# Optimization experiments

Hardware: AMD Instinct MI355X
Metric: run time of the kernel (lower is better)

Reference implementation:

```python
import jax, jax.numpy as jnp
import numpy as np

IN_F = 256
OUT_F = 128
ALPHA = 0.02  # LeakyReLU negative slope
NEG_INF = -9e15


def setup_inputs() -> dict:
    key = jax.random.key(0)
    ks = jax.random.split(key, 6)
    N = 8192
    x = jax.random.normal(ks[0], (N, IN_F), dtype=jnp.float32)
    adj = jax.random.randint(ks[1], (N, N), 0, 2, dtype=jnp.int32)
    # nn.Linear(in_feature, out_feature)
    lim1 = 1.0 / np.sqrt(IN_F)
    W1 = jax.random.uniform(ks[2], (IN_F, OUT_F), minval=-lim1, maxval=lim1, dtype=jnp.float32)
    b1 = jax.random.uniform(ks[3], (OUT_F,), minval=-lim1, maxval=lim1, dtype=jnp.float32)
    # nn.Linear(2*out_feature, 1)
    lim2 = 1.0 / np.sqrt(2 * OUT_F)
    a = jax.random.uniform(ks[4], (2 * OUT_F,), minval=-lim2, maxval=lim2, dtype=jnp.float32)
    b_att = jax.random.uniform(ks[5], (), minval=-lim2, maxval=lim2, dtype=jnp.float32)
    return {"x": x, "adj": adj, "W1": W1, "b1": b1, "a": a, "b_att": b_att}


def reference(x, adj, W1, b1, a, b_att):
    # Wh = weight1(x)  -> [N, F_out]
    Wh = x @ W1 + b1
    # att(cat(Wh_i, Wh_j)) = Wh_i @ a[:F] + Wh_j @ a[F:] + b  (no N^2*2F tensor)
    f_src = Wh @ a[:OUT_F]   # [N]
    f_dst = Wh @ a[OUT_F:]   # [N]
    e = f_src[:, None] + f_dst[None, :] + b_att          # [N, N]
    e = jnp.where(e > 0, e, ALPHA * e)                    # LeakyReLU
    scores = jnp.where(adj > 0, e, NEG_INF)
    attention = jax.nn.softmax(scores, axis=1)            # [N, N]
    # dropout is identity in eval mode (training=False)
    h_prime = attention @ Wh                               # [N, F_out]
    return jax.nn.elu(h_prime)                             # concat=True
```

## Files before the change

### kernel.cpp

```cpp
#include <hip/hip_runtime.h>
#include <hip/hip_bf16.h>

#define NODES 8192
#define INF_ 256
#define OUTF 128
#define LRALPHA 0.02f

typedef __bf16 bf16;
typedef bf16 bf16x4 __attribute__((ext_vector_type(4)));
typedef bf16 bf16x8 __attribute__((ext_vector_type(8)));
typedef float f32x4 __attribute__((ext_vector_type(4)));
typedef float f32x16 __attribute__((ext_vector_type(16)));
typedef int i32x4 __attribute__((ext_vector_type(4)));

__global__ __launch_bounds__(256) void gat_prep_r2(
    const float* __restrict__ x, const float* __restrict__ W1,
    const float* __restrict__ b1, const float* __restrict__ a,
    const float* __restrict__ b_att,
    bf16* __restrict__ WhbT, float* __restrict__ fsb, float* __restrict__ E1,
    float* __restrict__ E2, float* __restrict__ fd, float* __restrict__ F1,
    float* __restrict__ F2)
{
    __shared__ float xsT[64][36];
    __shared__ float ws1[64][132];
    __shared__ float wh[32][128];

    const int t = threadIdx.x;
    const int rbase = blockIdx.x * 32;
    const int tr = t >> 5;
    const int tc = t & 31;

    f32x4 acc[4];
    f32x4 bias = *(const f32x4*)&b1[tc * 4];
#pragma unroll
    for (int i = 0; i < 4; ++i) acc[i] = bias;

    for (int kt = 0; kt < 4; ++kt) {
        const int kb = kt * 64;
        {
            int r = t >> 3;
            int kq = (t & 7) * 8;
            f32x4 v0 = *(const f32x4*)&x[(size_t)(rbase + r) * INF_ + kb + kq];
            f32x4 v1 = *(const f32x4*)&x[(size_t)(rbase + r) * INF_ + kb + kq + 4];
#pragma unroll
            for (int i = 0; i < 4; ++i) xsT[kq + i][r] = v0[i];
#pragma unroll
            for (int i = 0; i < 4; ++i) xsT[kq + 4 + i][r] = v1[i];
        }
        {
            int kr = t >> 2;
            int cq = (t & 3) * 32;
#pragma unroll
            for (int i = 0; i < 8; ++i) {
                f32x4 v = *(const f32x4*)&W1[(size_t)(kb + kr) * OUTF + cq + i * 4];
                *(f32x4*)&ws1[kr][cq + i * 4] = v;
            }
        }
        __syncthreads();
        for (int kk = 0; kk < 64; ++kk) {
            f32x4 xa = *(const f32x4*)&xsT[kk][tr * 4];
            f32x4 wb = *(const f32x4*)&ws1[kk][tc * 4];
#pragma unroll
            for (int i = 0; i < 4; ++i)
#pragma unroll
                for (int j = 0; j < 4; ++j)
                    acc[i][j] += xa[i] * wb[j];
        }
        __syncthreads();
    }

#pragma unroll
    for (int i = 0; i < 4; ++i)
        *(f32x4*)&wh[tr * 4 + i][tc * 4] = acc[i];
    __syncthreads();

    if (t < 32) {
        float s1 = 0.f, s2 = 0.f;
        for (int c = 0; c < OUTF; ++c) {
            float v = wh[t][c];
            s1 += v * a[c];
            s2 += v * a[OUTF + c];
        }
        float fsv = s1 + b_att[0];
        int r = rbase + t;
        fsb[r] = fsv;
        E1[r] = expf(fsv);
        E2[r] = expf(LRALPHA * fsv);
        fd[r] = s2;
        F1[r] = expf(s2);
        F2[r] = expf(LRALPHA * s2);
    }

    {
        int c = t >> 1;
        int rr = (t & 1) * 16;
        bf16x8 b0, b1v;
#pragma unroll
        for (int i = 0; i < 8; ++i) b0[i] = (bf16)wh[rr + i][c];
#pragma unroll
        for (int i = 0; i < 8; ++i) b1v[i] = (bf16)wh[rr + 8 + i][c];
        *(bf16x8*)&WhbT[(size_t)c * NODES + rbase + rr] = b0;
        *(bf16x8*)&WhbT[(size_t)c * NODES + rbase + rr + 8] = b1v;
    }
}

#define SOFT_BAR() do { asm volatile("s_waitcnt lgkmcnt(0)" ::: "memory"); \
                        __builtin_amdgcn_s_barrier(); } while (0)

__global__ __launch_bounds__(1024, 4) void gat_attn_r2(
    const int* __restrict__ adj,
    const bf16* __restrict__ WhbT,
    const float* __restrict__ fsb, const float* __restrict__ E1,
    const float* __restrict__ E2, const float* __restrict__ fd,
    const float* __restrict__ F1, const float* __restrict__ F2,
    float* __restrict__ out)
{
    extern __shared__ char smem[];
    const int tid = threadIdx.x;
    const int wv = tid >> 6;
    const int lane = tid & 63;
    const int jg = wv >> 2;
    const int tt = wv & 3;
    const int rbase = blockIdx.x * 32;

    char* wbufA = smem + (jg * 2) * 4096;
    char* wbufB = smem + (jg * 2 + 1) * 4096;
    float* denred = (float*)(smem + 49152);

    const int r8 = lane >> 3;
    const int c8 = lane & 7;
    const int wrow = tt * 8 + r8;
    const int arow = lane & 31;
    const int ag = lane >> 5;

    const int gr = rbase + wrow;
    const float fsbv = fsb[gr];
    const float e1v = E1[gr];
    const float e2v = E2[gr];

    f32x16 acc;
#pragma unroll
    for (int i = 0; i < 16; ++i) acc[i] = 0.f;
    float den = 0.f;

    const int jw0 = jg * (NODES / 4);
    const size_t adj_row = (size_t)gr * NODES;
    const size_t whb_row = (size_t)(32 * tt + arow) * NODES;

    auto compute_w = [&](char* buf, int jb, i32x4 a0, i32x4 a1) {
        f32x4 fd0 = *(const f32x4*)&fd[jb + c8 * 8];
        f32x4 fd1 = *(const f32x4*)&fd[jb + c8 * 8 + 4];
        f32x4 g10 = *(const f32x4*)&F1[jb + c8 * 8];
        f32x4 g11 = *(const f32x4*)&F1[jb + c8 * 8 + 4];
        f32x4 g20 = *(const f32x4*)&F2[jb + c8 * 8];
        f32x4 g21 = *(const f32x4*)&F2[jb + c8 * 8 + 4];
        bf16x8 wb;
#pragma unroll
        for (int jj = 0; jj < 4; ++jj) {
            float s = fsbv + fd0[jj];
            bool pos = s > 0.f;
            float w = (pos ? e1v : e2v) * (pos ? g10[jj] : g20[jj]);
            w = a0[jj] ? w : 0.f;
            den += w;
            wb[jj] = (bf16)w;
        }
#pragma unroll
        for (int jj = 0; jj < 4; ++jj) {
            float s = fsbv + fd1[jj];
            bool pos = s > 0.f;
            float w = (pos ? e1v : e2v) * (pos ? g11[jj] : g21[jj]);
            w = a1[jj] ? w : 0.f;
            den += w;
            wb[4 + jj] = (bf16)w;
        }
        const int off = (wrow * 128 + c8 * 16) ^ ((wrow & 7) << 4);
        *(bf16x8*)(buf + off) = wb;
    };

    auto do_mfma = [&](const char* buf, int jb) {
        bf16x8 bfr[4];
#pragma unroll
        for (int m = 0; m < 4; ++m)
            bfr[m] = *(const bf16x8*)&WhbT[whb_row + jb + 16 * m + 8 * ag];
        bf16x8 af[4];
#pragma unroll
        for (int m = 0; m < 4; ++m) {
            const int aoff = (arow * 128 + m * 32 + ag * 16) ^ ((arow & 7) << 4);
            af[m] = *(const bf16x8*)(buf + aoff);
        }
#pragma unroll
        for (int m = 0; m < 4; ++m)
            acc = __builtin_amdgcn_mfma_f32_32x32x16_bf16(af[m], bfr[m], acc, 0, 0, 0);
    };

    i32x4 a0 = *(const i32x4*)&adj[adj_row + jw0 + c8 * 8];
    i32x4 a1 = *(const i32x4*)&adj[adj_row + jw0 + c8 * 8 + 4];
    i32x4 b0 = *(const i32x4*)&adj[adj_row + jw0 + 64 + c8 * 8];
    i32x4 b1 = *(const i32x4*)&adj[adj_row + jw0 + 64 + c8 * 8 + 4];
    compute_w(wbufA, jw0, a0, a1);
    SOFT_BAR();

    char* cur = wbufA;
    char* nxt = wbufB;
#pragma unroll 2
    for (int p = 0; p < 32; ++p) {
        const int jb = jw0 + p * 64;
        const int pc = (p + 2 <= 31) ? (p + 2) : 31;
        i32x4 n0 = *(const i32x4*)&adj[adj_row + jw0 + pc * 64 + c8 * 8];
        i32x4 n1 = *(const i32x4*)&adj[adj_row + jw0 + pc * 64 + c8 * 8 + 4];
        if (p < 31) compute_w(nxt, jb + 64, b0, b1);
        do_mfma(cur, jb);
        SOFT_BAR();
        b0 = n0; b1 = n1;
        char* tmp = cur; cur = nxt; nxt = tmp;
    }

    den += __shfl_xor(den, 1);
    den += __shfl_xor(den, 2);
    den += __shfl_xor(den, 4);
    if (c8 == 0) denred[jg * 32 + wrow] = den;

    if (jg > 0) {
        float* z = (float*)(smem + (size_t)((jg - 1) * 4 + tt) * 4096) + lane * 16;
        *(f32x16*)z = acc;
    }
    __syncthreads();

    if (jg == 0) {
#pragma unroll
        for (int q = 0; q < 3; ++q) {
            const float* z = (const float*)(smem + (size_t)(q * 4 + tt) * 4096) + lane * 16;
            f32x16 v = *(const f32x16*)z;
#pragma unroll
            for (int i = 0; i < 16; ++i) acc[i] += v[i];
        }
#pragma unroll
        for (int rg = 0; rg < 16; ++rg) {
            const int row = (rg & 3) + 8 * (rg >> 2) + 4 * ag;
            float ds = denred[row] + denred[32 + row] + denred[64 + row] + denred[96 + row];
            float v = acc[rg] / ds;
            v = v > 0.f ? v : expm1f(v);
            out[(size_t)(rbase + row) * OUTF + 32 * tt + arow] = v;
        }
    }
}

extern "C" void kernel_launch(void* const* d_in, const int* in_sizes, int n_in,
                              void* d_out, int out_size, void* d_ws, size_t ws_size,
                              hipStream_t stream) {
    const float* x     = (const float*)d_in[0];
    const int*   adj   = (const int*)d_in[1];
    const float* W1    = (const float*)d_in[2];
    const float* b1    = (const float*)d_in[3];
    const float* a     = (const float*)d_in[4];
    const float* b_att = (const float*)d_in[5];
    float* out = (float*)d_out;

    char* ws = (char*)d_ws;
    bf16* WhbT = (bf16*)ws;
    float* fsb = (float*)(ws + (size_t)2 * 1024 * 1024);
    float* E1 = fsb + NODES;
    float* E2 = E1 + NODES;
    float* fd = E2 + NODES;
    float* F1 = fd + NODES;
    float* F2 = F1 + NODES;

    hipLaunchKernelGGL(gat_prep_r2, dim3(NODES / 32), dim3(256), 0, stream,
                       x, W1, b1, a, b_att, WhbT, fsb, E1, E2, fd, F1, F2);

    const size_t smem2 = 49152 + 512;
    hipLaunchKernelGGL(gat_attn_r2, dim3(NODES / 32), dim3(1024), smem2, stream,
                       adj, WhbT, fsb, E1, E2, fd, F1, F2, out);
}
```

Measured before the change: 138.0 us.

## Stage F1/F2 tables in LDS, drop fd via algebra, prefetch WhbT fragments

```diff
diff --git a/kernel.cpp b/kernel.cpp
--- a/kernel.cpp
+++ b/kernel.cpp
@@ -13,7 +13,7 @@
 typedef float f32x16 __attribute__((ext_vector_type(16)));
 typedef int i32x4 __attribute__((ext_vector_type(4)));
 
-__global__ __launch_bounds__(256) void gat_prep_r2(
+__global__ __launch_bounds__(256) void gat_prep_r3(
     const float* __restrict__ x, const float* __restrict__ W1,
     const float* __restrict__ b1, const float* __restrict__ a,
     const float* __restrict__ b_att,
@@ -107,25 +107,41 @@
 #define SOFT_BAR() do { asm volatile("s_waitcnt lgkmcnt(0)" ::: "memory"); \
                         __builtin_amdgcn_s_barrier(); } while (0)
 
-__global__ __launch_bounds__(1024, 4) void gat_attn_r2(
+#define WBUF_OFF   0
+#define DENRED_OFF 32768
+#define F1T_OFF    33280
+#define F2T_OFF    66048
+#define ZONE_OFF   33280
+#define SMEM2_SIZE 98816
+
+__global__ __launch_bounds__(1024, 4) void gat_attn_r3(
     const int* __restrict__ adj,
     const bf16* __restrict__ WhbT,
     const float* __restrict__ fsb, const float* __restrict__ E1,
-    const float* __restrict__ E2, const float* __restrict__ fd,
+    const float* __restrict__ E2,
     const float* __restrict__ F1, const float* __restrict__ F2,
     float* __restrict__ out)
 {
     extern __shared__ char smem[];
     const int tid = threadIdx.x;
+    const int lane = tid & 63;
     const int wv = tid >> 6;
-    const int lane = tid & 63;
     const int jg = wv >> 2;
     const int tt = wv & 3;
     const int rbase = blockIdx.x * 32;
 
-    char* wbufA = smem + (jg * 2) * 4096;
-    char* wbufB = smem + (jg * 2 + 1) * 4096;
-    float* denred = (float*)(smem + 49152);
+    char* wbufA = smem + WBUF_OFF + (jg * 2) * 4096;
+    char* wbufB = smem + WBUF_OFF + (jg * 2 + 1) * 4096;
+    float* denred = (float*)(smem + DENRED_OFF);
+    float* F1t = (float*)(smem + F1T_OFF);
+    float* F2t = (float*)(smem + F2T_OFF);
+
+#pragma unroll
+    for (int it = 0; it < 2; ++it) {
+        int i = (it * 1024 + tid) * 4;
+        *(f32x4*)&F1t[i] = *(const f32x4*)&F1[i];
+        *(f32x4*)&F2t[i] = *(const f32x4*)&F2[i];
+    }
 
     const int r8 = lane >> 3;
     const int c8 = lane & 7;
@@ -147,56 +163,43 @@
     const size_t adj_row = (size_t)gr * NODES;
     const size_t whb_row = (size_t)(32 * tt + arow) * NODES;
 
+    __syncthreads();
+
     auto compute_w = [&](char* buf, int jb, i32x4 a0, i32x4 a1) {
-        f32x4 fd0 = *(const f32x4*)&fd[jb + c8 * 8];
-        f32x4 fd1 = *(const f32x4*)&fd[jb + c8 * 8 + 4];
-        f32x4 g10 = *(const f32x4*)&F1[jb + c8 * 8];
-        f32x4 g11 = *(const f32x4*)&F1[jb + c8 * 8 + 4];
-        f32x4 g20 = *(const f32x4*)&F2[jb + c8 * 8];
-        f32x4 g21 = *(const f32x4*)&F2[jb + c8 * 8 + 4];
+        const int cb = jb + c8 * 8;
+        f32x4 g10 = *(const f32x4*)&F1t[cb];
+        f32x4 g11 = *(const f32x4*)&F1t[cb + 4];
+        f32x4 g20 = *(const f32x4*)&F2t[cb];
+        f32x4 g21 = *(const f32x4*)&F2t[cb + 4];
         bf16x8 wb;
 #pragma unroll
         for (int jj = 0; jj < 4; ++jj) {
-            float s = fsbv + fd0[jj];
-            bool pos = s > 0.f;
-            float w = (pos ? e1v : e2v) * (pos ? g10[jj] : g20[jj]);
+            float t = e1v * g10[jj];
+            float w = t > 1.f ? t : e2v * g20[jj];
             w = a0[jj] ? w : 0.f;
             den += w;
             wb[jj] = (bf16)w;
         }
 #pragma unroll
         for (int jj = 0; jj < 4; ++jj) {
-            float s = fsbv + fd1[jj];
-            bool pos = s > 0.f;
-            float w = (pos ? e1v : e2v) * (pos ? g11[jj] : g21[jj]);
+            float t = e1v * g11[jj];
+            float w = t > 1.f ? t : e2v * g21[jj];
             w = a1[jj] ? w : 0.f;
             den += w;
             wb[4 + jj] = (bf16)w;
         }
         const int off = (wrow * 128 + c8 * 16) ^ ((wrow & 7) << 4);
         *(bf16x8*)(buf + off) = wb;
-    };
-
-    auto do_mfma = [&](const char* buf, int jb) {
-        bf16x8 bfr[4];
-#pragma unroll
-        for (int m = 0; m < 4; ++m)
-            bfr[m] = *(const bf16x8*)&WhbT[whb_row + jb + 16 * m + 8 * ag];
-        bf16x8 af[4];
-#pragma unroll
-        for (int m = 0; m < 4; ++m) {
-            const int aoff = (arow * 128 + m * 32 + ag * 16) ^ ((arow & 7) << 4);
-            af[m] = *(const bf16x8*)(buf + aoff);
-        }
-#pragma unroll
-        for (int m = 0; m < 4; ++m)
-            acc = __builtin_amdgcn_mfma_f32_32x32x16_bf16(af[m], bfr[m], acc, 0, 0, 0);
     };
 
     i32x4 a0 = *(const i32x4*)&adj[adj_row + jw0 + c8 * 8];
     i32x4 a1 = *(const i32x4*)&adj[adj_row + jw0 + c8 * 8 + 4];
     i32x4 b0 = *(const i32x4*)&adj[adj_row + jw0 + 64 + c8 * 8];
     i32x4 b1 = *(const i32x4*)&adj[adj_row + jw0 + 64 + c8 * 8 + 4];
+    bf16x8 wc0 = *(const bf16x8*)&WhbT[whb_row + jw0 + 0 + 8 * ag];
+    bf16x8 wc1 = *(const bf16x8*)&WhbT[whb_row + jw0 + 16 + 8 * ag];
+    bf16x8 wc2 = *(const bf16x8*)&WhbT[whb_row + jw0 + 32 + 8 * ag];
+    bf16x8 wc3 = *(const bf16x8*)&WhbT[whb_row + jw0 + 48 + 8 * ag];
     compute_w(wbufA, jw0, a0, a1);
     SOFT_BAR();
 
@@ -206,12 +209,36 @@
     for (int p = 0; p < 32; ++p) {
         const int jb = jw0 + p * 64;
         const int pc = (p + 2 <= 31) ? (p + 2) : 31;
+        const int pw = (p + 1 <= 31) ? (p + 1) : 31;
         i32x4 n0 = *(const i32x4*)&adj[adj_row + jw0 + pc * 64 + c8 * 8];
         i32x4 n1 = *(const i32x4*)&adj[adj_row + jw0 + pc * 64 + c8 * 8 + 4];
+        bf16x8 wn0 = *(const bf16x8*)&WhbT[whb_row + jw0 + pw * 64 + 0 + 8 * ag];
+        bf16x8 wn1 = *(const bf16x8*)&WhbT[whb_row + jw0 + pw * 64 + 16 + 8 * ag];
+        bf16x8 wn2 = *(const bf16x8*)&WhbT[whb_row + jw0 + pw * 64 + 32 + 8 * ag];
+        bf16x8 wn3 = *(const bf16x8*)&WhbT[whb_row + jw0 + pw * 64 + 48 + 8 * ag];
+
         if (p < 31) compute_w(nxt, jb + 64, b0, b1);
-        do_mfma(cur, jb);
+
+        {
+            bf16x8 af0, af1, af2, af3;
+            {
+                const int o0 = (arow * 128 + 0 * 32 + ag * 16) ^ ((arow & 7) << 4);
+                const int o1 = (arow * 128 + 1 * 32 + ag * 16) ^ ((arow & 7) << 4);
+                const int o2 = (arow * 128 + 2 * 32 + ag * 16) ^ ((arow & 7) << 4);
+                const int o3 = (arow * 128 + 3 * 32 + ag * 16) ^ ((arow & 7) << 4);
+                af0 = *(const bf16x8*)(cur + o0);
+                af1 = *(const bf16x8*)(cur + o1);
+                af2 = *(const bf16x8*)(cur + o2);
+                af3 = *(const bf16x8*)(cur + o3);
+            }
+            acc = __builtin_amdgcn_mfma_f32_32x32x16_bf16(af0, wc0, acc, 0, 0, 0);
+            acc = __builtin_amdgcn_mfma_f32_32x32x16_bf16(af1, wc1, acc, 0, 0, 0);
+            acc = __builtin_amdgcn_mfma_f32_32x32x16_bf16(af2, wc2, acc, 0, 0, 0);
+            acc = __builtin_amdgcn_mfma_f32_32x32x16_bf16(af3, wc3, acc, 0, 0, 0);
+        }
         SOFT_BAR();
         b0 = n0; b1 = n1;
+        wc0 = wn0; wc1 = wn1; wc2 = wn2; wc3 = wn3;
         char* tmp = cur; cur = nxt; nxt = tmp;
     }
 
@@ -221,7 +248,7 @@
     if (c8 == 0) denred[jg * 32 + wrow] = den;
 
     if (jg > 0) {
-        float* z = (float*)(smem + (size_t)((jg - 1) * 4 + tt) * 4096) + lane * 16;
+        float* z = (float*)(smem + ZONE_OFF + (size_t)((jg - 1) * 4 + tt) * 4096) + lane * 16;
         *(f32x16*)z = acc;
     }
     __syncthreads();
@@ -229,7 +256,7 @@
     if (jg == 0) {
 #pragma unroll
         for (int q = 0; q < 3; ++q) {
-            const float* z = (const float*)(smem + (size_t)(q * 4 + tt) * 4096) + lane * 16;
+            const float* z = (const float*)(smem + ZONE_OFF + (size_t)(q * 4 + tt) * 4096) + lane * 16;
             f32x16 v = *(const f32x16*)z;
 #pragma unroll
             for (int i = 0; i < 16; ++i) acc[i] += v[i];
@@ -265,10 +292,9 @@
     float* F1 = fd + NODES;
     float* F2 = F1 + NODES;
 
-    hipLaunchKernelGGL(gat_prep_r2, dim3(NODES / 32), dim3(256), 0, stream,
+    hipLaunchKernelGGL(gat_prep_r3, dim3(NODES / 32), dim3(256), 0, stream,
                        x, W1, b1, a, b_att, WhbT, fsb, E1, E2, fd, F1, F2);
 
-    const size_t smem2 = 49152 + 512;
-    hipLaunchKernelGGL(gat_attn_r2, dim3(NODES / 32), dim3(1024), smem2, stream,
-                       adj, WhbT, fsb, E1, E2, fd, F1, F2, out);
+    hipLaunchKernelGGL(gat_attn_r3, dim3(NODES / 32), dim3(1024), SMEM2_SIZE, stream,
+                       adj, WhbT, fsb, E1, E2, F1, F2, out);
 }
```

After: 120.1 us. 1.15x faster.

## Stage F1/F2 tables in LDS, double j-tile width, simplify LeakyReLU branch test

Applied to the files above, without the earlier changes.

```diff
diff --git a/kernel.cpp b/kernel.cpp
--- a/kernel.cpp
+++ b/kernel.cpp
@@ -13,13 +13,12 @@
 typedef float f32x16 __attribute__((ext_vector_type(16)));
 typedef int i32x4 __attribute__((ext_vector_type(4)));
 
-__global__ __launch_bounds__(256) void gat_prep_r2(
+__global__ __launch_bounds__(256) void gat_prep_r4(
     const float* __restrict__ x, const float* __restrict__ W1,
     const float* __restrict__ b1, const float* __restrict__ a,
     const float* __restrict__ b_att,
-    bf16* __restrict__ WhbT, float* __restrict__ fsb, float* __restrict__ E1,
-    float* __restrict__ E2, float* __restrict__ fd, float* __restrict__ F1,
-    float* __restrict__ F2)
+    bf16* __restrict__ WhbT, float* __restrict__ E1,
+    float* __restrict__ E2, float* __restrict__ F1, float* __restrict__ F2)
 {
     __shared__ float xsT[64][36];
     __shared__ float ws1[64][132];
@@ -83,10 +82,8 @@
         }
         float fsv = s1 + b_att[0];
         int r = rbase + t;
-        fsb[r] = fsv;
         E1[r] = expf(fsv);
         E2[r] = expf(LRALPHA * fsv);
-        fd[r] = s2;
         F1[r] = expf(s2);
         F2[r] = expf(LRALPHA * s2);
     }
@@ -107,25 +104,41 @@
 #define SOFT_BAR() do { asm volatile("s_waitcnt lgkmcnt(0)" ::: "memory"); \
                         __builtin_amdgcn_s_barrier(); } while (0)
 
-__global__ __launch_bounds__(1024, 4) void gat_attn_r2(
+#define WBUF_OFF   0
+#define DENRED_OFF 65536
+#define F1T_OFF    66048
+#define F2T_OFF    98816
+#define ZONE_OFF   66048
+#define SMEM2_SIZE 131584
+
+__global__ __launch_bounds__(1024, 4) void gat_attn_r4(
     const int* __restrict__ adj,
     const bf16* __restrict__ WhbT,
-    const float* __restrict__ fsb, const float* __restrict__ E1,
-    const float* __restrict__ E2, const float* __restrict__ fd,
+    const float* __restrict__ E1, const float* __restrict__ E2,
     const float* __restrict__ F1, const float* __restrict__ F2,
     float* __restrict__ out)
 {
     extern __shared__ char smem[];
     const int tid = threadIdx.x;
+    const int lane = tid & 63;
     const int wv = tid >> 6;
-    const int lane = tid & 63;
     const int jg = wv >> 2;
     const int tt = wv & 3;
     const int rbase = blockIdx.x * 32;
 
-    char* wbufA = smem + (jg * 2) * 4096;
-    char* wbufB = smem + (jg * 2 + 1) * 4096;
-    float* denred = (float*)(smem + 49152);
+    char* wbufA = smem + WBUF_OFF + jg * 16384;
+    char* wbufB = wbufA + 8192;
+    float* denred = (float*)(smem + DENRED_OFF);
+    float* F1t = (float*)(smem + F1T_OFF);
+    float* F2t = (float*)(smem + F2T_OFF);
+
+    {
+        int i = tid * 8;
+        *(f32x4*)&F1t[i]     = *(const f32x4*)&F1[i];
+        *(f32x4*)&F1t[i + 4] = *(const f32x4*)&F1[i + 4];
+        *(f32x4*)&F2t[i]     = *(const f32x4*)&F2[i];
+        *(f32x4*)&F2t[i + 4] = *(const f32x4*)&F2[i + 4];
+    }
 
     const int r8 = lane >> 3;
     const int c8 = lane & 7;
@@ -134,7 +147,6 @@
     const int ag = lane >> 5;
 
     const int gr = rbase + wrow;
-    const float fsbv = fsb[gr];
     const float e1v = E1[gr];
     const float e2v = E2[gr];
 
@@ -147,71 +159,70 @@
     const size_t adj_row = (size_t)gr * NODES;
     const size_t whb_row = (size_t)(32 * tt + arow) * NODES;
 
-    auto compute_w = [&](char* buf, int jb, i32x4 a0, i32x4 a1) {
-        f32x4 fd0 = *(const f32x4*)&fd[jb + c8 * 8];
-        f32x4 fd1 = *(const f32x4*)&fd[jb + c8 * 8 + 4];
-        f32x4 g10 = *(const f32x4*)&F1[jb + c8 * 8];
-        f32x4 g11 = *(const f32x4*)&F1[jb + c8 * 8 + 4];
-        f32x4 g20 = *(const f32x4*)&F2[jb + c8 * 8];
-        f32x4 g21 = *(const f32x4*)&F2[jb + c8 * 8 + 4];
-        bf16x8 wb;
-#pragma unroll
-        for (int jj = 0; jj < 4; ++jj) {
-            float s = fsbv + fd0[jj];
-            bool pos = s > 0.f;
-            float w = (pos ? e1v : e2v) * (pos ? g10[jj] : g20[jj]);
-            w = a0[jj] ? w : 0.f;
-            den += w;
-            wb[jj] = (bf16)w;
-        }
-#pragma unroll
-        for (int jj = 0; jj < 4; ++jj) {
-            float s = fsbv + fd1[jj];
-            bool pos = s > 0.f;
-            float w = (pos ? e1v : e2v) * (pos ? g11[jj] : g21[jj]);
-            w = a1[jj] ? w : 0.f;
-            den += w;
-            wb[4 + jj] = (bf16)w;
-        }
-        const int off = (wrow * 128 + c8 * 16) ^ ((wrow & 7) << 4);
-        *(bf16x8*)(buf + off) = wb;
+    __syncthreads();
+
+    auto compute_w = [&](char* buf, int jb, const i32x4* av) {
+        const int cb = jb + c8 * 16;
+#pragma unroll
+        for (int h = 0; h < 2; ++h) {
+            bf16x8 wb;
+#pragma unroll
+            for (int q = 0; q < 2; ++q) {
+                f32x4 g1 = *(const f32x4*)&F1t[cb + h * 8 + q * 4];
+                f32x4 g2 = *(const f32x4*)&F2t[cb + h * 8 + q * 4];
+                i32x4 am = av[h * 2 + q];
+#pragma unroll
+                for (int jj = 0; jj < 4; ++jj) {
+                    float tv = e1v * g1[jj];
+                    float w = tv > 1.f ? tv : e2v * g2[jj];
+                    w = am[jj] ? w : 0.f;
+                    den += w;
+                    wb[q * 4 + jj] = (bf16)w;
+                }
+            }
+            const int off = (wrow * 256 + c8 * 32 + h * 16) ^ ((wrow & 7) << 4);
+            *(bf16x8*)(buf + off) = wb;
+        }
     };
 
-    auto do_mfma = [&](const char* buf, int jb) {
-        bf16x8 bfr[4];
-#pragma unroll
-        for (int m = 0; m < 4; ++m)
-            bfr[m] = *(const bf16x8*)&WhbT[whb_row + jb + 16 * m + 8 * ag];
-        bf16x8 af[4];
-#pragma unroll
-        for (int m = 0; m < 4; ++m) {
-            const int aoff = (arow * 128 + m * 32 + ag * 16) ^ ((arow & 7) << 4);
-            af[m] = *(const bf16x8*)(buf + aoff);
-        }
-#pragma unroll
-        for (int m = 0; m < 4; ++m)
-            acc = __builtin_amdgcn_mfma_f32_32x32x16_bf16(af[m], bfr[m], acc, 0, 0, 0);
-    };
-
-    i32x4 a0 = *(const i32x4*)&adj[adj_row + jw0 + c8 * 8];
-    i32x4 a1 = *(const i32x4*)&adj[adj_row + jw0 + c8 * 8 + 4];
-    i32x4 b0 = *(const i32x4*)&adj[adj_row + jw0 + 64 + c8 * 8];
-    i32x4 b1 = *(const i32x4*)&adj[adj_row + jw0 + 64 + c8 * 8 + 4];
-    compute_w(wbufA, jw0, a0, a1);
+    i32x4 ca[4], na[4];
+#pragma unroll
+    for (int q = 0; q < 4; ++q)
+        ca[q] = *(const i32x4*)&adj[adj_row + jw0 + c8 * 16 + q * 4];
+#pragma unroll
+    for (int q = 0; q < 4; ++q)
+        na[q] = *(const i32x4*)&adj[adj_row + jw0 + 128 + c8 * 16 + q * 4];
+    compute_w(wbufA, jw0, ca);
     SOFT_BAR();
 
     char* cur = wbufA;
     char* nxt = wbufB;
 #pragma unroll 2
-    for (int p = 0; p < 32; ++p) {
-        const int jb = jw0 + p * 64;
-        const int pc = (p + 2 <= 31) ? (p + 2) : 31;
-        i32x4 n0 = *(const i32x4*)&adj[adj_row + jw0 + pc * 64 + c8 * 8];
-        i32x4 n1 = *(const i32x4*)&adj[adj_row + jw0 + pc * 64 + c8 * 8 + 4];
-        if (p < 31) compute_w(nxt, jb + 64, b0, b1);
-        do_mfma(cur, jb);
+    for (int p = 0; p < 16; ++p) {
+        const int jb = jw0 + p * 128;
+
+        bf16x8 wc[8];
+#pragma unroll
+        for (int m = 0; m < 8; ++m)
+            wc[m] = *(const bf16x8*)&WhbT[whb_row + jb + 16 * m + 8 * ag];
+
+        const int pc = (p + 2 <= 15) ? (p + 2) : 15;
+        i32x4 fa[4];
+#pragma unroll
+        for (int q = 0; q < 4; ++q)
+            fa[q] = *(const i32x4*)&adj[adj_row + jw0 + pc * 128 + c8 * 16 + q * 4];
+
+        if (p < 15) compute_w(nxt, jb + 128, na);
+
+#pragma unroll
+        for (int m = 0; m < 8; ++m) {
+            const int aoff = (arow * 256 + m * 32 + ag * 16) ^ ((arow & 7) << 4);
+            bf16x8 af = *(const bf16x8*)(cur + aoff);
+            acc = __builtin_amdgcn_mfma_f32_32x32x16_bf16(af, wc[m], acc, 0, 0, 0);
+        }
         SOFT_BAR();
-        b0 = n0; b1 = n1;
+#pragma unroll
+        for (int q = 0; q < 4; ++q) { na[q] = fa[q]; }
         char* tmp = cur; cur = nxt; nxt = tmp;
     }
 
@@ -221,7 +232,7 @@
     if (c8 == 0) denred[jg * 32 + wrow] = den;
 
     if (jg > 0) {
-        float* z = (float*)(smem + (size_t)((jg - 1) * 4 + tt) * 4096) + lane * 16;
+        float* z = (float*)(smem + ZONE_OFF + (size_t)((jg - 1) * 4 + tt) * 4096) + lane * 16;
         *(f32x16*)z = acc;
     }
     __syncthreads();
@@ -229,7 +240,7 @@
     if (jg == 0) {
 #pragma unroll
         for (int q = 0; q < 3; ++q) {
-            const float* z = (const float*)(smem + (size_t)(q * 4 + tt) * 4096) + lane * 16;
+            const float* z = (const float*)(smem + ZONE_OFF + (size_t)(q * 4 + tt) * 4096) + lane * 16;
             f32x16 v = *(const f32x16*)z;
 #pragma unroll
             for (int i = 0; i < 16; ++i) acc[i] += v[i];
@@ -258,17 +269,14 @@
 
     char* ws = (char*)d_ws;
     bf16* WhbT = (bf16*)ws;
-    float* fsb = (float*)(ws + (size_t)2 * 1024 * 1024);
-    float* E1 = fsb + NODES;
+    float* E1 = (float*)(ws + (size_t)2 * 1024 * 1024);
     float* E2 = E1 + NODES;
-    float* fd = E2 + NODES;
-    float* F1 = fd + NODES;
+    float* F1 = E2 + NODES;
     float* F2 = F1 + NODES;
 
-    hipLaunchKernelGGL(gat_prep_r2, dim3(NODES / 32), dim3(256), 0, stream,
-                       x, W1, b1, a, b_att, WhbT, fsb, E1, E2, fd, F1, F2);
-
-    const size_t smem2 = 49152 + 512;
-    hipLaunchKernelGGL(gat_attn_r2, dim3(NODES / 32), dim3(1024), smem2, stream,
-                       adj, WhbT, fsb, E1, E2, fd, F1, F2, out);
+    hipLaunchKernelGGL(gat_prep_r4, dim3(NODES / 32), dim3(256), 0, stream,
+                       x, W1, b1, a, b_att, WhbT, E1, E2, F1, F2);
+
+    hipLaunchKernelGGL(gat_attn_r4, dim3(NODES / 32), dim3(1024), SMEM2_SIZE, stream,
+                       adj, WhbT, E1, E2, F1, F2, out);
 }
```

Measured after the change: 126.7 us. 1.09x faster.
